# Kernel tuning notes

Measured on AMD Instinct MI355X. Metric: run time of the kernel, lower is better.

## Reference

```python
import jax, jax.numpy as jnp
from jax import lax
import numpy as np

V, D, H, K = 50000, 300, 256, 37  # vocab, emb dim, lstm hidden, num_tags
B, T = 64, 256


def setup_inputs() -> dict:
    key = jax.random.key(0)
    ks = jax.random.split(key, 24)
    lengths = jax.random.randint(ks[0], (B,), T // 2, T + 1)
    valid = jnp.arange(T)[None, :] < lengths[:, None]
    text = jnp.where(valid, jax.random.randint(ks[1], (B, T), 1, V), 0)
    sbj = jax.random.randint(ks[2], (B, T), 0, K)

    def p(k, shape, s=0.05):
        return jax.random.normal(k, shape, jnp.float32) * s

    return {
        "text": text, "sbj": sbj,
        "emb": p(ks[3], (V, D), 0.1),
        # layer 0 (input D=300), forward + backward directions, torch gate order i,f,g,o
        "Wih0f": p(ks[4], (4 * H, D)), "Whh0f": p(ks[5], (4 * H, H)), "b0f": jnp.zeros((4 * H,), jnp.float32),
        "Wih0b": p(ks[6], (4 * H, D)), "Whh0b": p(ks[7], (4 * H, H)), "b0b": jnp.zeros((4 * H,), jnp.float32),
        # layer 1 (input 2H=512)
        "Wih1f": p(ks[8], (4 * H, 2 * H)), "Whh1f": p(ks[9], (4 * H, H)), "b1f": jnp.zeros((4 * H,), jnp.float32),
        "Wih1b": p(ks[10], (4 * H, 2 * H)), "Whh1b": p(ks[11], (4 * H, H)), "b1b": jnp.zeros((4 * H,), jnp.float32),
        "W_sbj": p(ks[12], (K, 2 * H)), "b_sbj": jnp.zeros((K,), jnp.float32),
        # CRF params (torchcrf init: uniform(-0.1, 0.1))
        "start_t": p(ks[13], (K,), 0.1), "end_t": p(ks[14], (K,), 0.1), "trans": p(ks[15], (K, K), 0.1),
    }


def _lstm(x, Wih, Whh, b, reverse):
    # x: [T, B, Din] time-major; returns hidden states [T, B, H]
    Bn, Hn = x.shape[1], Whh.shape[1]

    def step(carry, xt):
        h, c = carry
        z = xt @ Wih.T + h @ Whh.T + b
        i, f, g, o = jnp.split(z, 4, axis=-1)
        c = jax.nn.sigmoid(f) * c + jax.nn.sigmoid(i) * jnp.tanh(g)
        h = jax.nn.sigmoid(o) * jnp.tanh(c)
        return (h, c), h

    init = (jnp.zeros((Bn, Hn), x.dtype), jnp.zeros((Bn, Hn), x.dtype))
    return lax.scan(step, init, x, reverse=reverse)[1]


def reference(text, sbj, emb, Wih0f, Whh0f, b0f, Wih0b, Whh0b, b0b,
              Wih1f, Whh1f, b1f, Wih1b, Whh1b, b1b,
              W_sbj, b_sbj, start_t, end_t, trans):
    mask = (text != 0)                      # [B, T]
    x = jnp.transpose(emb[text], (1, 0, 2))  # [T, B, D]
    h0 = jnp.concatenate([_lstm(x, Wih0f, Whh0f, b0f, False),
                          _lstm(x, Wih0b, Whh0b, b0b, True)], axis=-1)   # [T, B, 2H]
    h1 = jnp.concatenate([_lstm(h0, Wih1f, Whh1f, b1f, False),
                          _lstm(h0, Wih1b, Whh1b, b1b, True)], axis=-1)  # [T, B, 2H]
    em = h1 @ W_sbj.T + b_sbj               # emissions [T, B, K]

    tags = sbj.T                            # [T, B]
    m = mask.T                              # [T, B]
    mf = m.astype(em.dtype)

    # --- numerator: score of the gold path ---
    em_sel = jnp.take_along_axis(em, tags[:, :, None], axis=2)[..., 0]  # [T, B]
    tr_sel = trans[tags[:-1], tags[1:]]                                  # [T-1, B]
    seq_ends = m.sum(0) - 1
    last_tags = tags[seq_ends, jnp.arange(tags.shape[1])]
    num = (start_t[tags[0]] + em_sel[0]
           + jnp.sum((em_sel[1:] + tr_sel) * mf[1:], axis=0)
           + end_t[last_tags])              # [B]

    # --- log partition: forward algorithm (logsumexp DP over K tags) ---
    def step(score, inp):
        em_t, m_t = inp
        nxt = jax.scipy.special.logsumexp(
            score[:, :, None] + trans[None, :, :] + em_t[:, None, :], axis=1)
        return jnp.where(m_t[:, None], nxt, score), None

    score0 = start_t[None, :] + em[0]       # [B, K]
    score = lax.scan(step, score0, (em[1:], m[1:]))[0]
    logZ = jax.scipy.special.logsumexp(score + end_t[None, :], axis=-1)  # [B]

    llh = num - logZ
    return -(llh.sum() / mf.sum())          # -1 * token_mean log-likelihood
```

## Files before the change

### kernel.cpp

```cpp
#include <hip/hip_runtime.h>
#include <math.h>

#define TT 256
#define BB 64
#define DD 300
#define KP0 320
#define HH 256
#define KK 37
#define FH 1024
#define MTOT (TT*BB)

typedef __attribute__((ext_vector_type(8))) short short8;
typedef __attribute__((ext_vector_type(4))) float f32x4;

__device__ __forceinline__ float bf2f(unsigned short u) {
    union { float f; unsigned int i; } v; v.i = ((unsigned int)u) << 16; return v.f;
}
__device__ __forceinline__ unsigned short f2bf(float f) {
    union { float f; unsigned int i; } v; v.f = f;
    unsigned int i = v.i;
    unsigned int r = (i + 0x7FFFu + ((i >> 16) & 1u)) >> 16;
    return (unsigned short)r;
}
__device__ __forceinline__ float sigm(float x)   { return 1.0f / (1.0f + __expf(-x)); }
__device__ __forceinline__ float tanh_f(float x) { return 2.0f / (1.0f + __expf(-2.0f * x)) - 1.0f; }

__device__ __forceinline__ int sb0(int w) { return (w << 24) >> 24; }
__device__ __forceinline__ int sb1(int w) { return (w << 16) >> 24; }
__device__ __forceinline__ int sb2(int w) { return (w <<  8) >> 24; }
__device__ __forceinline__ int sb3(int w) { return  w        >> 24; }

#if defined(__has_builtin)
#if __has_builtin(__builtin_amdgcn_sdot4)
#define HAVE_SDOT4 1
#endif
#endif

__device__ __forceinline__ int dot4i8(int a, int b, int c) {
#ifdef HAVE_SDOT4
    return __builtin_amdgcn_sdot4(a, b, c, false);
#else
    return c + sb0(a) * sb0(b) + sb1(a) * sb1(b) + sb2(a) * sb2(b) + sb3(a) * sb3(b);
#endif
}

__device__ __forceinline__ void lstm_dot(int hw, int4 wv, int& a0, int& a1, int& a2, int& a3) {
    a0 = dot4i8(hw, wv.x, a0);
    a1 = dot4i8(hw, wv.y, a1);
    a2 = dot4i8(hw, wv.z, a2);
    a3 = dot4i8(hw, wv.w, a3);
}

__device__ __forceinline__ int perm_col(int nn) { return ((nn & 255) << 2) | (nn >> 8); }

__global__ __launch_bounds__(64) void conv_scale(
    const float* __restrict__ w0f, const float* __restrict__ w0b,
    const float* __restrict__ w1f, const float* __restrict__ w1b,
    float* __restrict__ S)
{
    const int m = blockIdx.x >> 10;
    const int r = blockIdx.x & 1023;
    const float* W = m == 0 ? w0f : m == 1 ? w0b : m == 2 ? w1f : w1b;
    const int t = threadIdx.x;
    float mx = 0.f;
    for (int k = t; k < HH; k += 64) mx = fmaxf(mx, fabsf(W[r * HH + k]));
    #pragma unroll
    for (int s = 32; s > 0; s >>= 1) mx = fmaxf(mx, __shfl_down(mx, s, 64));
    if (t == 0) {
        const int g = r >> 8, u = r & 255;
        S[m * 1024 + u * 4 + g] = fmaxf(mx, 1e-20f) / 127.0f;
    }
}

__global__ __launch_bounds__(256) void conv_wq(
    const float* __restrict__ w0f, const float* __restrict__ w0b,
    const float* __restrict__ w1f, const float* __restrict__ w1b,
    const float* __restrict__ S, unsigned int* __restrict__ WQ)
{
    const int idx = blockIdx.x * 256 + threadIdx.x;
    const int m = idx >> 16;
    const int r = idx & 65535;
    const float* W = m == 0 ? w0f : m == 1 ? w0b : m == 2 ? w1f : w1b;
    const int g  = r & 3;
    const int u  = (r >> 2) & 255;
    const int j  = (r >> 10) & 15;
    const int kq = r >> 14;
    const int k0 = kq * 64 + j * 4;
    const float s = S[m * 1024 + u * 4 + g];
    const float4 wv = *(const float4*)(W + (g * HH + u) * HH + k0);
    int q0 = (int)rintf(wv.x / s), q1 = (int)rintf(wv.y / s);
    int q2 = (int)rintf(wv.z / s), q3 = (int)rintf(wv.w / s);
    q0 = max(-127, min(127, q0)); q1 = max(-127, min(127, q1));
    q2 = max(-127, min(127, q2)); q3 = max(-127, min(127, q3));
    WQ[idx] = (unsigned int)(q0 & 0xff) | ((unsigned int)(q1 & 0xff) << 8) |
              ((unsigned int)(q2 & 0xff) << 16) | ((unsigned int)(q3 & 0xff) << 24);
}

__global__ __launch_bounds__(256) void conv_wsbj_bf(
    const float* __restrict__ Wsbj, unsigned short* __restrict__ WB)
{
    const int idx = blockIdx.x * 256 + threadIdx.x;
    if (idx >= 64 * 512) return;
    const int r = idx >> 9, cidx = idx & 511;
    WB[idx] = (r < KK) ? f2bf(Wsbj[r * 512 + cidx]) : (unsigned short)0;
}

__global__ __launch_bounds__(320) void conv_gather(
    const int* __restrict__ text, const float* __restrict__ emb,
    unsigned short* __restrict__ Abf)
{
    const int r = blockIdx.x;
    const int k = threadIdx.x;
    const int t = r >> 6, b = r & 63;
    const int idx = text[b * TT + t];
    Abf[r * KP0 + k] = (k < DD) ? f2bf(emb[(size_t)idx * DD + k]) : (unsigned short)0;
}

__global__ __launch_bounds__(256) void conv_w(
    const float* __restrict__ src, unsigned short* __restrict__ dst,
    int kin, int kout, int total)
{
    const int idx = blockIdx.x * 256 + threadIdx.x;
    if (idx >= total) return;
    const int rr = idx / kout, k = idx - rr * kout;
    dst[idx] = (k < kin) ? f2bf(src[rr * kin + k]) : (unsigned short)0;
}

__global__ __launch_bounds__(256) void gemm_mfma2(
    const unsigned short* __restrict__ A,
    const unsigned short* __restrict__ Wf,
    const unsigned short* __restrict__ Wb,
    const float* __restrict__ biasf,
    const float* __restrict__ biasb,
    unsigned short* __restrict__ outf,
    unsigned short* __restrict__ outb,
    int lda)
{
    const unsigned short* W = blockIdx.z ? Wb : Wf;
    const float* bias        = blockIdx.z ? biasb : biasf;
    unsigned short* out      = blockIdx.z ? outb : outf;

    const int bm = blockIdx.x * 128;
    const int bn = blockIdx.y * 128;
    const int tid = threadIdx.x;
    const int lane = tid & 63;
    const int wave = tid >> 6;
    const int wm = (wave & 1) * 64;
    const int wn = (wave >> 1) * 64;

    __shared__ __align__(16) unsigned short As[128 * 32];
    __shared__ __align__(16) unsigned short Bs[128 * 32];

    f32x4 acc[4][4] = {};

    const int srow = tid >> 2;
    const int sk = (tid & 3) * 8;

    const unsigned short* ga0 = A + (size_t)(bm + srow) * lda + sk;
    const unsigned short* ga1 = A + (size_t)(bm + srow + 64) * lda + sk;
    const unsigned short* gb0 = W + (size_t)(bn + srow) * lda + sk;
    const unsigned short* gb1 = W + (size_t)(bn + srow + 64) * lda + sk;

    unsigned short* lA0 = As + wave * 512;
    unsigned short* lA1 = As + 2048 + wave * 512;
    unsigned short* lB0 = Bs + wave * 512;
    unsigned short* lB1 = Bs + 2048 + wave * 512;

    const int kiters = lda >> 5;
    for (int kb = 0; kb < kiters; kb++) {
        const int k0 = kb * 32;
        __builtin_amdgcn_global_load_lds(
            (const __attribute__((address_space(1))) unsigned int*)(ga0 + k0),
            (__attribute__((address_space(3))) unsigned int*)lA0, 16, 0, 0);
        __builtin_amdgcn_global_load_lds(
            (const __attribute__((address_space(1))) unsigned int*)(ga1 + k0),
            (__attribute__((address_space(3))) unsigned int*)lA1, 16, 0, 0);
        __builtin_amdgcn_global_load_lds(
            (const __attribute__((address_space(1))) unsigned int*)(gb0 + k0),
            (__attribute__((address_space(3))) unsigned int*)lB0, 16, 0, 0);
        __builtin_amdgcn_global_load_lds(
            (const __attribute__((address_space(1))) unsigned int*)(gb1 + k0),
            (__attribute__((address_space(3))) unsigned int*)lB1, 16, 0, 0);
        __syncthreads();

        short8 af[4], bfr[4];
        #pragma unroll
        for (int i = 0; i < 4; i++) {
            af[i]  = *(const short8*)&As[(wm + i * 16 + (lane & 15)) * 32 + (lane >> 4) * 8];
            bfr[i] = *(const short8*)&Bs[(wn + i * 16 + (lane & 15)) * 32 + (lane >> 4) * 8];
        }
        #pragma unroll
        for (int i = 0; i < 4; i++)
            #pragma unroll
            for (int j = 0; j < 4; j++)
                acc[i][j] = __builtin_amdgcn_mfma_f32_16x16x32_bf16(af[i], bfr[j], acc[i][j], 0, 0, 0);
        __syncthreads();
    }

    const int cn = lane & 15;
    const int cr = (lane >> 4) * 4;
    #pragma unroll
    for (int j = 0; j < 4; j++) {
        const int n = bn + wn + j * 16 + cn;
        const float bv = bias[n];
        const int pc = perm_col(n);
        #pragma unroll
        for (int i = 0; i < 4; i++) {
            #pragma unroll
            for (int r = 0; r < 4; r++) {
                const int m = bm + wm + i * 16 + cr + r;
                out[(size_t)m * FH + pc] = f2bf(acc[i][j][r] + bv);
            }
        }
    }
}

__global__ __launch_bounds__(256) void gemm_em(
    const unsigned short* __restrict__ A,
    const unsigned short* __restrict__ W,
    const float* __restrict__ bias,
    float* __restrict__ em)
{
    const int bm = blockIdx.x * 128;
    const int tid = threadIdx.x;
    const int lane = tid & 63;
    const int wave = tid >> 6;
    const int wm = (wave & 1) * 64;
    const int wn = (wave >> 1) * 32;

    __shared__ __align__(16) unsigned short As[128 * 32];
    __shared__ __align__(16) unsigned short Bs[64 * 32];

    f32x4 acc[4][2] = {};

    const int srow = tid >> 2;
    const int sk = (tid & 3) * 8;

    const unsigned short* ga0 = A + (size_t)(bm + srow) * 512 + sk;
    const unsigned short* ga1 = A + (size_t)(bm + srow + 64) * 512 + sk;
    const unsigned short* gb  = W + (size_t)srow * 512 + sk;

    unsigned short* lA0 = As + wave * 512;
    unsigned short* lA1 = As + 2048 + wave * 512;
    unsigned short* lB  = Bs + wave * 512;

    for (int kb = 0; kb < 16; kb++) {
        const int k0 = kb * 32;
        __builtin_amdgcn_global_load_lds(
            (const __attribute__((address_space(1))) unsigned int*)(ga0 + k0),
            (__attribute__((address_space(3))) unsigned int*)lA0, 16, 0, 0);
        __builtin_amdgcn_global_load_lds(
            (const __attribute__((address_space(1))) unsigned int*)(ga1 + k0),
            (__attribute__((address_space(3))) unsigned int*)lA1, 16, 0, 0);
        __builtin_amdgcn_global_load_lds(
            (const __attribute__((address_space(1))) unsigned int*)(gb + k0),
            (__attribute__((address_space(3))) unsigned int*)lB, 16, 0, 0);
        __syncthreads();

        short8 af[4], bfr[2];
        #pragma unroll
        for (int i = 0; i < 4; i++)
            af[i]  = *(const short8*)&As[(wm + i * 16 + (lane & 15)) * 32 + (lane >> 4) * 8];
        #pragma unroll
        for (int j = 0; j < 2; j++)
            bfr[j] = *(const short8*)&Bs[(wn + j * 16 + (lane & 15)) * 32 + (lane >> 4) * 8];
        #pragma unroll
        for (int i = 0; i < 4; i++)
            #pragma unroll
            for (int j = 0; j < 2; j++)
                acc[i][j] = __builtin_amdgcn_mfma_f32_16x16x32_bf16(af[i], bfr[j], acc[i][j], 0, 0, 0);
        __syncthreads();
    }

    const int cn = lane & 15;
    const int cr = (lane >> 4) * 4;
    #pragma unroll
    for (int j = 0; j < 2; j++) {
        const int n = wn + j * 16 + cn;
        if (n < KK) {
            const float bv = bias[n];
            #pragma unroll
            for (int i = 0; i < 4; i++) {
                #pragma unroll
                for (int r = 0; r < 4; r++) {
                    const int m = bm + wm + i * 16 + cr + r;
                    em[(size_t)m * KK + n] = acc[i][j][r] + bv;
                }
            }
        }
    }
}

__global__ __launch_bounds__(1024, 4) void lstm_kernel(
    const unsigned short* __restrict__ zin_f, const unsigned short* __restrict__ zin_b,
    const int* __restrict__ WQf, const int* __restrict__ WQb,
    const float* __restrict__ Sf, const float* __restrict__ Sb,
    unsigned short* __restrict__ h_out)
{
    const int dir = blockIdx.y;
    const unsigned short* zin = dir ? zin_b : zin_f;
    const int*   WQ = dir ? WQb : WQf;
    const float* S  = dir ? Sb  : Sf;
    const int off = dir ? HH : 0;

    const int b = blockIdx.x;
    const int tid = threadIdx.x;
    const int u  = tid & 255;
    const int kq = tid >> 8;

    __shared__ __align__(16) unsigned char hq8[2][HH];
    __shared__ int4 red[3][HH];

    const int4* wp = (const int4*)WQ + kq * 16 * 256 + u;
    const int4 w0  = wp[ 0 * 256], w1  = wp[ 1 * 256], w2  = wp[ 2 * 256], w3  = wp[ 3 * 256];
    const int4 w4  = wp[ 4 * 256], w5  = wp[ 5 * 256], w6  = wp[ 6 * 256], w7  = wp[ 7 * 256];
    const int4 w8  = wp[ 8 * 256], w9  = wp[ 9 * 256], w10 = wp[10 * 256], w11 = wp[11 * 256];
    const int4 w12 = wp[12 * 256], w13 = wp[13 * 256], w14 = wp[14 * 256], w15 = wp[15 * 256];

    float4 sc = make_float4(0.f, 0.f, 0.f, 0.f);
    if (kq == 0) {
        sc = *(const float4*)(S + 4 * u);
        const float inv127 = 1.0f / 127.0f;
        sc.x *= inv127; sc.y *= inv127; sc.z *= inv127; sc.w *= inv127;
    }
    float c = 0.0f;
    int cur = 0;
    if (tid < 128) ((unsigned int*)hq8)[tid] = 0u;
    __syncthreads();

    for (int ts = 0; ts < TT; ts++) {
        const int tt = dir ? (TT - 1 - ts) : ts;
        const int row = tt * BB + b;

        ushort4 zv = make_ushort4(0, 0, 0, 0);
        if (kq == 0) zv = *(const ushort4*)(zin + row * FH + 4 * u);

        const int4* hv = (const int4*)&hq8[cur][kq * 64];
        const int4 hA = hv[0], hB = hv[1], hC = hv[2], hD = hv[3];

        int a0 = 0, a1 = 0, a2 = 0, a3 = 0;
        lstm_dot(hA.x, w0,  a0, a1, a2, a3);
        lstm_dot(hA.y, w1,  a0, a1, a2, a3);
        lstm_dot(hA.z, w2,  a0, a1, a2, a3);
        lstm_dot(hA.w, w3,  a0, a1, a2, a3);
        lstm_dot(hB.x, w4,  a0, a1, a2, a3);
        lstm_dot(hB.y, w5,  a0, a1, a2, a3);
        lstm_dot(hB.z, w6,  a0, a1, a2, a3);
        lstm_dot(hB.w, w7,  a0, a1, a2, a3);
        lstm_dot(hC.x, w8,  a0, a1, a2, a3);
        lstm_dot(hC.y, w9,  a0, a1, a2, a3);
        lstm_dot(hC.z, w10, a0, a1, a2, a3);
        lstm_dot(hC.w, w11, a0, a1, a2, a3);
        lstm_dot(hD.x, w12, a0, a1, a2, a3);
        lstm_dot(hD.y, w13, a0, a1, a2, a3);
        lstm_dot(hD.z, w14, a0, a1, a2, a3);
        lstm_dot(hD.w, w15, a0, a1, a2, a3);

        if (kq) red[kq - 1][u] = make_int4(a0, a1, a2, a3);
        __syncthreads();

        if (kq == 0) {
            const int4 r0 = red[0][u], r1 = red[1][u], r2 = red[2][u];
            const int A0 = a0 + r0.x + r1.x + r2.x;
            const int A1 = a1 + r0.y + r1.y + r2.y;
            const int A2 = a2 + r0.z + r1.z + r2.z;
            const int A3 = a3 + r0.w + r1.w + r2.w;
            const float zi  = (float)A0 * sc.x + bf2f(zv.x);
            const float zf_ = (float)A1 * sc.y + bf2f(zv.y);
            const float zg  = (float)A2 * sc.z + bf2f(zv.z);
            const float zo  = (float)A3 * sc.w + bf2f(zv.w);
            const float cc = sigm(zf_) * c + sigm(zi) * tanh_f(zg);
            c = cc;
            const float hh = sigm(zo) * tanh_f(cc);
            hq8[cur ^ 1][u] = (unsigned char)((int)rintf(hh * 127.0f));
            h_out[row * (2 * HH) + off + u] = f2bf(hh);
        }
        __syncthreads();
        cur ^= 1;
    }
}

__global__ __launch_bounds__(64) void crf_kernel(
    const int* __restrict__ text, const int* __restrict__ sbj,
    const float* __restrict__ em,
    const float* __restrict__ start_t, const float* __restrict__ end_t,
    const float* __restrict__ trans, float* __restrict__ accum)
{
    const int b = blockIdx.x;
    const int tid = threadIdx.x;
    __shared__ float tr[KK * KK];
    __shared__ float sc[2][KK];
    for (int x = tid; x < KK * KK; x += 64) tr[x] = trans[x];

    int cnt = 0;
    for (int t = tid; t < TT; t += 64) cnt += (text[b * TT + t] != 0) ? 1 : 0;
    #pragma unroll
    for (int s = 32; s > 0; s >>= 1) cnt += __shfl_down(cnt, s, 64);
    const int len = __shfl(cnt, 0, 64);

    __syncthreads();

    float part = 0.f;
    for (int t = tid; t < TT; t += 64) {
        if (t >= 1 && t < len) {
            const int tg = sbj[b * TT + t];
            const int tp = sbj[b * TT + t - 1];
            part += em[(t * BB + b) * KK + tg] + tr[tp * KK + tg];
        }
    }
    #pragma unroll
    for (int s = 32; s > 0; s >>= 1) part += __shfl_down(part, s, 64);

    if (tid < KK) sc[0][tid] = start_t[tid] + em[b * KK + tid];
    __syncthreads();
    int cur = 0;
    for (int t = 1; t < len; t++) {
        float nv = 0.f;
        if (tid < KK) {
            float mx = -1e30f;
            for (int k1 = 0; k1 < KK; k1++)
                mx = fmaxf(mx, sc[cur][k1] + tr[k1 * KK + tid]);
            float s = 0.f;
            for (int k1 = 0; k1 < KK; k1++)
                s += __expf(sc[cur][k1] + tr[k1 * KK + tid] - mx);
            nv = mx + __logf(s) + em[(t * BB + b) * KK + tid];
        }
        if (tid < KK) sc[cur ^ 1][tid] = nv;
        __syncthreads();
        cur ^= 1;
    }

    if (tid == 0) {
        const int tg0 = sbj[b * TT];
        const int tgl = sbj[b * TT + len - 1];
        const float num = start_t[tg0] + em[b * KK + tg0] + part + end_t[tgl];
        float mx = -1e30f;
        for (int k = 0; k < KK; k++) mx = fmaxf(mx, sc[cur][k] + end_t[k]);
        float s = 0.f;
        for (int k = 0; k < KK; k++) s += __expf(sc[cur][k] + end_t[k] - mx);
        const float logZ = mx + __logf(s);
        atomicAdd(&accum[0], num - logZ);
        atomicAdd(&accum[1], (float)len);
    }
}

__global__ void init_kernel(float* __restrict__ accum) {
    if (threadIdx.x < 2) accum[threadIdx.x] = 0.0f;
}
__global__ void final_kernel(const float* __restrict__ accum, float* __restrict__ out) {
    out[0] = -(accum[0] / accum[1]);
}

extern "C" void kernel_launch(void* const* d_in, const int* in_sizes, int n_in,
                              void* d_out, int out_size, void* d_ws, size_t ws_size,
                              hipStream_t stream)
{
    (void)in_sizes; (void)n_in; (void)out_size; (void)ws_size;
    const int*   text  = (const int*)d_in[0];
    const int*   sbj   = (const int*)d_in[1];
    const float* emb   = (const float*)d_in[2];
    const float* Wih0f = (const float*)d_in[3];
    const float* Whh0f = (const float*)d_in[4];
    const float* b0f   = (const float*)d_in[5];
    const float* Wih0b = (const float*)d_in[6];
    const float* Whh0b = (const float*)d_in[7];
    const float* b0b   = (const float*)d_in[8];
    const float* Wih1f = (const float*)d_in[9];
    const float* Whh1f = (const float*)d_in[10];
    const float* b1f   = (const float*)d_in[11];
    const float* Wih1b = (const float*)d_in[12];
    const float* Whh1b = (const float*)d_in[13];
    const float* b1b   = (const float*)d_in[14];
    const float* Wsbj  = (const float*)d_in[15];
    const float* bsbj  = (const float*)d_in[16];
    const float* start_t = (const float*)d_in[17];
    const float* end_t   = (const float*)d_in[18];
    const float* trans   = (const float*)d_in[19];

    char* ws = (char*)d_ws;
    unsigned short* zf   = (unsigned short*)(ws + 0);
    unsigned short* zb   = (unsigned short*)(ws + 33554432);
    unsigned short* h0   = (unsigned short*)(ws + 67108864);
    unsigned short* h1   = (unsigned short*)(ws + 83886080);
    unsigned short* Wb0f = (unsigned short*)(ws + 67108864);
    unsigned short* Wb0b = (unsigned short*)(ws + 67764224);
    unsigned short* Abf  = (unsigned short*)(ws + 83886080);
    unsigned short* Wb1f = (unsigned short*)(ws + 94371840);
    unsigned short* Wb1b = (unsigned short*)(ws + 95420416);
    unsigned int*   WQ   = (unsigned int*)(ws + 100663296);
    float*          Sq   = (float*)(ws + 101711872);
    unsigned short* WsbjB = (unsigned short*)(ws + 102760448);
    float*          acc  = (float*)(ws + 102836224);
    float*           em  = (float*)(ws + 0);
    float* out = (float*)d_out;

    const int* WQ0f = (const int*)(WQ + 0 * 65536);
    const int* WQ0b = (const int*)(WQ + 1 * 65536);
    const int* WQ1f = (const int*)(WQ + 2 * 65536);
    const int* WQ1b = (const int*)(WQ + 3 * 65536);
    const float* S0f = Sq + 0 * 1024;
    const float* S0b = Sq + 1 * 1024;
    const float* S1f = Sq + 2 * 1024;
    const float* S1b = Sq + 3 * 1024;

    init_kernel<<<1, 64, 0, stream>>>(acc);
    conv_scale<<<dim3(4096), 64, 0, stream>>>(Whh0f, Whh0b, Whh1f, Whh1b, Sq);
    conv_wq<<<dim3(1024), 256, 0, stream>>>(Whh0f, Whh0b, Whh1f, Whh1b, Sq, WQ);
    conv_wsbj_bf<<<dim3(128), 256, 0, stream>>>(Wsbj, WsbjB);
    conv_gather<<<dim3(MTOT), 320, 0, stream>>>(text, emb, Abf);
    conv_w<<<dim3(1280), 256, 0, stream>>>(Wih0f, Wb0f, DD, KP0, 1024 * KP0);
    conv_w<<<dim3(1280), 256, 0, stream>>>(Wih0b, Wb0b, DD, KP0, 1024 * KP0);
    conv_w<<<dim3(2048), 256, 0, stream>>>(Wih1f, Wb1f, 512, 512, 1024 * 512);
    conv_w<<<dim3(2048), 256, 0, stream>>>(Wih1b, Wb1b, 512, 512, 1024 * 512);

    gemm_mfma2<<<dim3(128, 8, 2), 256, 0, stream>>>(Abf, Wb0f, Wb0b, b0f, b0b, zf, zb, KP0);
    lstm_kernel<<<dim3(BB, 2), 1024, 0, stream>>>(zf, zb, WQ0f, WQ0b, S0f, S0b, h0);
    gemm_mfma2<<<dim3(128, 8, 2), 256, 0, stream>>>(h0, Wb1f, Wb1b, b1f, b1b, zf, zb, 512);
    lstm_kernel<<<dim3(BB, 2), 1024, 0, stream>>>(zf, zb, WQ1f, WQ1b, S1f, S1b, h1);

    gemm_em<<<dim3(128), 256, 0, stream>>>(h1, WsbjB, bsbj, em);
    crf_kernel<<<BB, 64, 0, stream>>>(text, sbj, em, start_t, end_t, trans, acc);
    final_kernel<<<1, 1, 0, stream>>>(acc, out);
}
```

Measured before the change: 1.018 ms.

## Prefetch LSTM gate inputs, use LDS-only barriers, register-cache CRF transitions, merge weight conversions

The LSTM recurrence now loads the next timestep's precomputed gate inputs one iteration ahead, so the global load latency overlaps the dot products. Its __syncthreads calls become an inline s_waitcnt lgkmcnt(0) plus s_barrier, which waits only on LDS traffic and does not drain outstanding global stores. The CRF forward loop keeps its transition column in registers and computes the scores once per step instead of twice. The four input-weight bf16 conversion launches are merged into one 2D launch, which adds some idle blocks for the smaller matrices.

```diff
diff --git a/kernel.cpp b/kernel.cpp
--- a/kernel.cpp
+++ b/kernel.cpp
@@ -49,6 +49,10 @@
     a1 = dot4i8(hw, wv.y, a1);
     a2 = dot4i8(hw, wv.z, a2);
     a3 = dot4i8(hw, wv.w, a3);
+}
+
+__device__ __forceinline__ void barrier_lgkm() {
+    asm volatile("s_waitcnt lgkmcnt(0)\n\ts_barrier" ::: "memory");
 }
 
 __device__ __forceinline__ int perm_col(int nn) { return ((nn & 255) << 2) | (nn >> 8); }
@@ -116,10 +120,18 @@
     Abf[r * KP0 + k] = (k < DD) ? f2bf(emb[(size_t)idx * DD + k]) : (unsigned short)0;
 }
 
-__global__ __launch_bounds__(256) void conv_w(
-    const float* __restrict__ src, unsigned short* __restrict__ dst,
-    int kin, int kout, int total)
-{
+__global__ __launch_bounds__(256) void conv_w4(
+    const float* __restrict__ s0, const float* __restrict__ s1,
+    const float* __restrict__ s2, const float* __restrict__ s3,
+    unsigned short* __restrict__ d0, unsigned short* __restrict__ d1,
+    unsigned short* __restrict__ d2, unsigned short* __restrict__ d3)
+{
+    const int z = blockIdx.y;
+    const float* src = z == 0 ? s0 : z == 1 ? s1 : z == 2 ? s2 : s3;
+    unsigned short* dst = z == 0 ? d0 : z == 1 ? d1 : z == 2 ? d2 : d3;
+    const int kin   = z < 2 ? DD  : 512;
+    const int kout  = z < 2 ? KP0 : 512;
+    const int total = 1024 * kout;
     const int idx = blockIdx.x * 256 + threadIdx.x;
     if (idx >= total) return;
     const int rr = idx / kout, k = idx - rr * kout;
@@ -328,12 +340,22 @@
     if (tid < 128) ((unsigned int*)hq8)[tid] = 0u;
     __syncthreads();
 
+    ushort4 zv = make_ushort4(0, 0, 0, 0);
+    if (kq == 0) {
+        const int tt0 = dir ? (TT - 1) : 0;
+        zv = *(const ushort4*)(zin + (tt0 * BB + b) * FH + 4 * u);
+    }
+
     for (int ts = 0; ts < TT; ts++) {
         const int tt = dir ? (TT - 1 - ts) : ts;
         const int row = tt * BB + b;
 
-        ushort4 zv = make_ushort4(0, 0, 0, 0);
-        if (kq == 0) zv = *(const ushort4*)(zin + row * FH + 4 * u);
+        ushort4 zv_n = make_ushort4(0, 0, 0, 0);
+        if (kq == 0) {
+            const int ts_n = (ts + 1 < TT) ? (ts + 1) : ts;
+            const int tt_n = dir ? (TT - 1 - ts_n) : ts_n;
+            zv_n = *(const ushort4*)(zin + (tt_n * BB + b) * FH + 4 * u);
+        }
 
         const int4* hv = (const int4*)&hq8[cur][kq * 64];
         const int4 hA = hv[0], hB = hv[1], hC = hv[2], hD = hv[3];
@@ -357,7 +379,7 @@
         lstm_dot(hD.w, w15, a0, a1, a2, a3);
 
         if (kq) red[kq - 1][u] = make_int4(a0, a1, a2, a3);
-        __syncthreads();
+        barrier_lgkm();
 
         if (kq == 0) {
             const int4 r0 = red[0][u], r1 = red[1][u], r2 = red[2][u];
@@ -375,8 +397,9 @@
             hq8[cur ^ 1][u] = (unsigned char)((int)rintf(hh * 127.0f));
             h_out[row * (2 * HH) + off + u] = f2bf(hh);
         }
-        __syncthreads();
+        barrier_lgkm();
         cur ^= 1;
+        zv = zv_n;
     }
 }
 
@@ -411,19 +434,29 @@
     #pragma unroll
     for (int s = 32; s > 0; s >>= 1) part += __shfl_down(part, s, 64);
 
+    float tc[KK];
+    #pragma unroll
+    for (int k1 = 0; k1 < KK; k1++) tc[k1] = (tid < KK) ? tr[k1 * KK + tid] : 0.f;
+
     if (tid < KK) sc[0][tid] = start_t[tid] + em[b * KK + tid];
     __syncthreads();
     int cur = 0;
     for (int t = 1; t < len; t++) {
         float nv = 0.f;
         if (tid < KK) {
+            const float ev = em[(t * BB + b) * KK + tid];
+            float v[KK];
             float mx = -1e30f;
+            #pragma unroll
+            for (int k1 = 0; k1 < KK; k1++) {
+                v[k1] = sc[cur][k1] + tc[k1];
+                mx = fmaxf(mx, v[k1]);
+            }
+            float s = 0.f;
+            #pragma unroll
             for (int k1 = 0; k1 < KK; k1++)
-                mx = fmaxf(mx, sc[cur][k1] + tr[k1 * KK + tid]);
-            float s = 0.f;
-            for (int k1 = 0; k1 < KK; k1++)
-                s += __expf(sc[cur][k1] + tr[k1 * KK + tid] - mx);
-            nv = mx + __logf(s) + em[(t * BB + b) * KK + tid];
+                s += __expf(v[k1] - mx);
+            nv = mx + __logf(s) + ev;
         }
         if (tid < KK) sc[cur ^ 1][tid] = nv;
         __syncthreads();
@@ -508,10 +541,8 @@
     conv_wq<<<dim3(1024), 256, 0, stream>>>(Whh0f, Whh0b, Whh1f, Whh1b, Sq, WQ);
     conv_wsbj_bf<<<dim3(128), 256, 0, stream>>>(Wsbj, WsbjB);
     conv_gather<<<dim3(MTOT), 320, 0, stream>>>(text, emb, Abf);
-    conv_w<<<dim3(1280), 256, 0, stream>>>(Wih0f, Wb0f, DD, KP0, 1024 * KP0);
-    conv_w<<<dim3(1280), 256, 0, stream>>>(Wih0b, Wb0b, DD, KP0, 1024 * KP0);
-    conv_w<<<dim3(2048), 256, 0, stream>>>(Wih1f, Wb1f, 512, 512, 1024 * 512);
-    conv_w<<<dim3(2048), 256, 0, stream>>>(Wih1b, Wb1b, 512, 512, 1024 * 512);
+    conv_w4<<<dim3(2048, 4), 256, 0, stream>>>(Wih0f, Wih0b, Wih1f, Wih1b,
+                                               Wb0f, Wb0b, Wb1f, Wb1b);
 
     gemm_mfma2<<<dim3(128, 8, 2), 256, 0, stream>>>(Abf, Wb0f, Wb0b, b0f, b0b, zf, zb, KP0);
     lstm_kernel<<<dim3(BB, 2), 1024, 0, stream>>>(zf, zb, WQ0f, WQ0b, S0f, S0b, h0);
```

Result: faster. 968.9 us (-4.8%).
